# Performance work log

Measured on AMD Instinct MI355X. Metric: run time of the kernel, lower is better.

The kernel has to match this reference:

```python
import jax, jax.numpy as jnp
import numpy as np

N_NODES = 50000
N_EDGES = 800000
IN_FEAT = 128
HEADS = 4
UNITS = 16
LEAKY_ALPHA = 0.2  # tf.nn.leaky_relu default


def setup_inputs() -> dict:
    key = jax.random.key(0)
    k1, k2, k3, k4, k5 = jax.random.split(key, 5)
    x = jax.random.normal(k1, (N_NODES, IN_FEAT), dtype=jnp.float32)
    edge_index = jax.random.randint(k2, (N_EDGES, 2), 0, N_NODES, dtype=jnp.int32)
    # Dense kernel (glorot-ish scaling), no bias (use_bias=False)
    W = jax.random.normal(k3, (IN_FEAT, HEADS * UNITS), dtype=jnp.float32) * (1.0 / np.sqrt(IN_FEAT))
    glorot = np.sqrt(2.0 / (1 + UNITS)).astype(np.float32)
    att_w1 = jax.random.normal(k4, (HEADS, 1, UNITS), dtype=jnp.float32) * glorot
    att_w2 = jax.random.normal(k5, (HEADS, 1, UNITS), dtype=jnp.float32) * glorot
    return {"x": x, "edge_index": edge_index, "W": W, "att_w1": att_w1, "att_w2": att_w2}


def reference(x, edge_index, W, att_w1, att_w2):
    n_nodes = x.shape[0]
    h = x @ W  # [N, H*U]
    snd_idx = edge_index[:, 0]
    rcv_idx = edge_index[:, 1]
    # gather per-edge features, split into heads -> [H, E, U]
    sender = h[snd_idx].reshape(-1, HEADS, UNITS).transpose(1, 0, 2)
    receiver = h[rcv_idx].reshape(-1, HEADS, UNITS).transpose(1, 0, 2)
    # per-edge, per-head attention logits [H, E]
    att = jnp.sum(att_w1 * sender, axis=-1) + jnp.sum(att_w2 * receiver, axis=-1)
    att = jnp.where(att > 0, att, LEAKY_ALPHA * att)
    # segment softmax over receiver neighborhoods, per head
    seg_max = jax.vmap(lambda a: jax.ops.segment_max(a, rcv_idx, num_segments=n_nodes))(att)  # [H, N]
    e = jnp.exp(att - seg_max[:, rcv_idx])
    denom = jax.vmap(lambda a: jax.ops.segment_sum(a, rcv_idx, num_segments=n_nodes))(e)  # [H, N]
    alpha = e / denom[:, rcv_idx]  # [H, E]
    # weighted scatter-sum of sender features -> [H, N, U]
    out = jax.vmap(lambda v: jax.ops.segment_sum(v, rcv_idx, num_segments=n_nodes))(sender * alpha[:, :, None])
    # concat heads -> [N, H*U]; activation is None (identity)
    return out.transpose(1, 0, 2).reshape(n_nodes, HEADS * UNITS)
```

## Files before the change

kernel.cpp:

```cpp
#include <hip/hip_runtime.h>
#include <math.h>

#define N_NODES 50000
#define N_EDGES 800000
#define IN_FEAT 128
#define HEADS   4
#define UNITS   16
#define OUTF    64
#define LEAKY   0.2f

#define NB      196
#define BCAP    5120
#define CAP     64
#define GEMM_BLKS 782
#define A_BLOCKS  391
#define EPB     8

typedef __attribute__((ext_vector_type(8))) short bf16x8;
typedef __attribute__((ext_vector_type(4))) float f32x4;

__device__ __forceinline__ unsigned short f2bf(float f) {
    unsigned u = __float_as_uint(f);
    unsigned r = u + 0x7FFFu + ((u >> 16) & 1u);
    return (unsigned short)(r >> 16);
}
__device__ __forceinline__ float bf2f(unsigned short b) {
    return __uint_as_float(((unsigned)b) << 16);
}

union SharedU {
    struct { unsigned short wt[64 * 136]; } g;
    struct { int2 stage[2048]; int hist[256], cur[256], adj[256], wsum[4]; } a;
};

__global__ __launch_bounds__(256) void prep(const float* __restrict__ W,
                                            const float* __restrict__ w1,
                                            const float* __restrict__ w2,
                                            unsigned short* __restrict__ Wt_g,
                                            unsigned short* __restrict__ Wea_g,
                                            int* __restrict__ bucket_cnt) {
    int idx = blockIdx.x * 256 + threadIdx.x;
    if (idx < NB) bucket_cnt[idx] = 0;
    if (idx < IN_FEAT * OUTF) {
        int k = idx >> 6, c = idx & 63;
        Wt_g[c * IN_FEAT + k] = f2bf(W[idx]);
    }
    if (idx < IN_FEAT * HEADS) {
        int k = idx >> 2, hd = idx & 3;
        float s1 = 0.f, s2 = 0.f;
        #pragma unroll
        for (int u = 0; u < UNITS; ++u) {
            float wv = W[k * OUTF + hd * UNITS + u];
            s1 += wv * w1[hd * UNITS + u];
            s2 += wv * w2[hd * UNITS + u];
        }
        unsigned short h1 = f2bf(s1), h2 = f2bf(s2);
        unsigned short l1 = f2bf(s1 - bf2f(h1)), l2 = f2bf(s2 - bf2f(h2));
        Wea_g[(hd)      * IN_FEAT + k] = h1;
        Wea_g[(4 + hd)  * IN_FEAT + k] = h2;
        Wea_g[(8 + hd)  * IN_FEAT + k] = l1;
        Wea_g[(12 + hd) * IN_FEAT + k] = l2;
    }
}

__global__ __launch_bounds__(256, 4) void fused_gemm_bucketA(const float* __restrict__ x,
                                                             const unsigned short* __restrict__ Wt_g,
                                                             const unsigned short* __restrict__ Wea_g,
                                                             const int2* __restrict__ ei,
                                                             unsigned short* __restrict__ hg,
                                                             float* __restrict__ a1,
                                                             float* __restrict__ a2,
                                                             int* __restrict__ bucket_cnt,
                                                             int2* __restrict__ buckets) {
    __shared__ SharedU sh;
    const int t = threadIdx.x;
    const int lane = t & 63, wv = t >> 6;

    if (blockIdx.x >= GEMM_BLKS) {
        const int e0 = (blockIdx.x - GEMM_BLKS) * 2048;
        sh.a.hist[t] = 0;
        __syncthreads();

        int2 ed[EPB]; int bk[EPB];
        #pragma unroll
        for (int j = 0; j < EPB; ++j) {
            int e = e0 + t + j * 256;
            if (e < N_EDGES) {
                ed[j] = ei[e];
                bk[j] = ed[j].y >> 8;
                atomicAdd(&sh.a.hist[bk[j]], 1);
            } else bk[j] = -1;
        }
        __syncthreads();
        const int v = sh.a.hist[t];
        int inc = v;
        #pragma unroll
        for (int off = 1; off < 64; off <<= 1) {
            int u = __shfl_up(inc, off, 64);
            if (lane >= off) inc += u;
        }
        if (lane == 63) sh.a.wsum[wv] = inc;
        __syncthreads();
        const int s0 = sh.a.wsum[0], s1 = sh.a.wsum[1], s2 = sh.a.wsum[2];
        const int wo = (wv > 0 ? s0 : 0) + (wv > 1 ? s1 : 0) + (wv > 2 ? s2 : 0);
        const int excl = wo + inc - v;
        sh.a.cur[t] = excl;
        if (t < NB) {
            int g0 = atomicAdd(&bucket_cnt[t], v);
            sh.a.adj[t] = g0 - excl;
        }
        __syncthreads();
        #pragma unroll
        for (int j = 0; j < EPB; ++j) {
            if (bk[j] >= 0) {
                int p = atomicAdd(&sh.a.cur[bk[j]], 1);
                sh.a.stage[p] = ed[j];
            }
        }
        __syncthreads();
        const int total = min(2048, N_EDGES - e0);
        for (int i = t; i < total; i += 256) {
            int2 vv = sh.a.stage[i];
            int b = vv.y >> 8;
            buckets[(size_t)(b * BCAP + sh.a.adj[b] + i)] = vv;
        }
        return;
    }

    const int node0 = blockIdx.x * 64;
    unsigned short* wt = sh.g.wt;

    {
        const ushort4* Wt4 = (const ushort4*)Wt_g;
        #pragma unroll
        for (int it = 0; it < 8; ++it) {
            int idx = t + 256 * it;
            int c = idx >> 5, u = idx & 31;
            *(ushort4*)&wt[c * 136 + u * 4] = Wt4[idx];
        }
    }
    __syncthreads();

    const int m = lane & 15, quad = lane >> 4;
    const int n0 = wv * 16;
    const int arow = min(node0 + n0 + m, N_NODES - 1);
    const float* xr = x + (size_t)arow * IN_FEAT;

    f32x4 acc[4] = {{0,0,0,0},{0,0,0,0},{0,0,0,0},{0,0,0,0}};
    f32x4 acca   = {0,0,0,0};
    #pragma unroll
    for (int kc = 0; kc < 4; ++kc) {
        float4 v0 = *(const float4*)(xr + kc * 32 + quad * 8);
        float4 v1 = *(const float4*)(xr + kc * 32 + quad * 8 + 4);
        bf16x8 af;
        af[0] = (short)f2bf(v0.x); af[1] = (short)f2bf(v0.y);
        af[2] = (short)f2bf(v0.z); af[3] = (short)f2bf(v0.w);
        af[4] = (short)f2bf(v1.x); af[5] = (short)f2bf(v1.y);
        af[6] = (short)f2bf(v1.z); af[7] = (short)f2bf(v1.w);
        #pragma unroll
        for (int ct = 0; ct < 4; ++ct) {
            bf16x8 bfr = *(bf16x8*)&wt[(ct * 16 + m) * 136 + kc * 32 + quad * 8];
            acc[ct] = __builtin_amdgcn_mfma_f32_16x16x32_bf16(af, bfr, acc[ct], 0, 0, 0);
        }
        bf16x8 waf = *(const bf16x8*)(Wea_g + (size_t)m * IN_FEAT + kc * 32 + quad * 8);
        acca = __builtin_amdgcn_mfma_f32_16x16x32_bf16(af, waf, acca, 0, 0, 0);
    }

    #pragma unroll
    for (int r = 0; r < 4; ++r) {
        float vres = acca[r] + __shfl_xor(acca[r], 8, 64);
        int node = node0 + n0 + quad * 4 + r;
        if (node < N_NODES) {
            if (m < 4)      a1[node * 4 + m]       = vres;
            else if (m < 8) a2[node * 4 + (m - 4)] = vres;
        }
    }

    __syncthreads();
    unsigned short* hl = sh.g.wt;
    #pragma unroll
    for (int ct = 0; ct < 4; ++ct)
        #pragma unroll
        for (int r = 0; r < 4; ++r)
            hl[(n0 + quad * 4 + r) * 72 + ct * 16 + m] = f2bf(acc[ct][r]);
    __syncthreads();
    #pragma unroll
    for (int it = 0; it < 2; ++it) {
        int u = t + 256 * it;
        int r = u >> 3, cg = u & 7;
        int node = node0 + r;
        if (node < N_NODES)
            *(uint4*)&hg[(size_t)node * OUTF + cg * 8] = *(uint4*)&hl[r * 72 + cg * 8];
    }
}

__global__ __launch_bounds__(1024) void bucketB(const int2* __restrict__ buckets,
                                                const int* __restrict__ bucket_cnt,
                                                int* __restrict__ csr,
                                                int* __restrict__ deg) {
    __shared__ int snds[BCAP];
    __shared__ int hist[256], cur[256], strt[256], wsum[4];
    const int b = blockIdx.x;
    const int t = threadIdx.x;
    const int cnt = bucket_cnt[b];
    if (t < 256) hist[t] = 0;
    __syncthreads();
    for (int i = t; i < cnt; i += 1024)
        atomicAdd(&hist[buckets[(size_t)b * BCAP + i].y & 255], 1);
    __syncthreads();
    int v = 0, inc = 0;
    if (t < 256) {
        const int lane = t & 63, wvx = t >> 6;
        v = hist[t];
        inc = v;
        #pragma unroll
        for (int off = 1; off < 64; off <<= 1) {
            int u = __shfl_up(inc, off, 64);
            if (lane >= off) inc += u;
        }
        if (lane == 63) wsum[wvx] = inc;
    }
    __syncthreads();
    if (t < 256) {
        const int wvx = t >> 6;
        const int s0 = wsum[0], s1 = wsum[1], s2 = wsum[2];
        const int wo = (wvx > 0 ? s0 : 0) + (wvx > 1 ? s1 : 0) + (wvx > 2 ? s2 : 0);
        const int excl = wo + inc - v;
        strt[t] = excl;
        cur[t]  = excl;
        const int node = b * 256 + t;
        if (node < N_NODES) deg[node] = v;
    }
    __syncthreads();
    for (int i = t; i < cnt; i += 1024) {
        int2 vv = buckets[(size_t)b * BCAP + i];
        int p = atomicAdd(&cur[vv.y & 255], 1);
        snds[p] = vv.x;
    }
    __syncthreads();
    for (int u = t; u < 256 * CAP; u += 1024) {
        const int loc = u >> 6, slot = u & (CAP - 1);
        const int d = hist[loc];
        const int val = (d > 0) ? snds[strt[loc] + min(slot, d - 1)] : 0;
        csr[(size_t)b * (256 * CAP) + u] = val;
    }
}

__global__ __launch_bounds__(256, 8) void gather_kernel(const int* __restrict__ deg,
                                                        const int* __restrict__ csr,
                                                        const float* __restrict__ a1,
                                                        const float* __restrict__ a2,
                                                        const unsigned short* __restrict__ h,
                                                        float* __restrict__ out) {
    const int wave = threadIdx.x >> 6;
    const int lane = threadIdx.x & 63;
    const int n = blockIdx.x * 4 + wave;
    if (n >= N_NODES) return;
    const int sv = csr[(size_t)n * CAP + lane];
    const int cn = min(deg[n], CAP);
    const int sub  = lane >> 3;
    const int li   = lane & 7;
    const int head = li >> 1;
    if (cn <= 0) {
        if (sub == 0) {
            *(float4*)(out + (size_t)n * OUTF + li * 8)     = make_float4(0.f, 0.f, 0.f, 0.f);
            *(float4*)(out + (size_t)n * OUTF + li * 8 + 4) = make_float4(0.f, 0.f, 0.f, 0.f);
        }
        return;
    }
    const float a2h = a2[n * 4 + head];
    const uint4* h4 = (const uint4*)h;

    float acc[8] = {0.f,0.f,0.f,0.f,0.f,0.f,0.f,0.f};
    float den = 0.f;

    for (int i0 = 0; i0 < cn; i0 += 16) {
        #pragma unroll
        for (int g = 0; g < 2; ++g) {
            int er = i0 + g * 8 + sub;
            int ec = min(er, cn - 1);
            int s = __shfl(sv, ec, 64);
            float t0 = a1[s * 4 + head] + a2h;
            t0 = t0 > 0.f ? t0 : LEAKY * t0;
            float e = (er < cn) ? __expf(t0) : 0.f;
            uint4 hv = h4[(unsigned)(s * 8 + li)];
            const unsigned hw[4] = {hv.x, hv.y, hv.z, hv.w};
            #pragma unroll
            for (int q = 0; q < 4; ++q) {
                acc[q*2+0] = fmaf(e, __uint_as_float(hw[q] << 16),         acc[q*2+0]);
                acc[q*2+1] = fmaf(e, __uint_as_float(hw[q] & 0xFFFF0000u), acc[q*2+1]);
            }
            den += e;
        }
    }

    #pragma unroll
    for (int off = 8; off <= 32; off <<= 1) {
        #pragma unroll
        for (int q = 0; q < 8; ++q) acc[q] += __shfl_xor(acc[q], off, 64);
        den += __shfl_xor(den, off, 64);
    }

    if (sub == 0) {
        float inv = 1.f / den;
        *(float4*)(out + (size_t)n * OUTF + li * 8) =
            make_float4(acc[0] * inv, acc[1] * inv, acc[2] * inv, acc[3] * inv);
        *(float4*)(out + (size_t)n * OUTF + li * 8 + 4) =
            make_float4(acc[4] * inv, acc[5] * inv, acc[6] * inv, acc[7] * inv);
    }
}

extern "C" void kernel_launch(void* const* d_in, const int* in_sizes, int n_in,
                              void* d_out, int out_size, void* d_ws, size_t ws_size,
                              hipStream_t stream) {
    const float* x  = (const float*)d_in[0];
    const int2*  ei = (const int2*)d_in[1];
    const float* W  = (const float*)d_in[2];
    const float* w1 = (const float*)d_in[3];
    const float* w2 = (const float*)d_in[4];
    float* out = (float*)d_out;

    unsigned short* h    = (unsigned short*)d_ws;
    float* a1            = (float*)(h + (size_t)N_NODES * OUTF);
    float* a2            = a1 + (size_t)N_NODES * HEADS;
    unsigned short* Wt_g = (unsigned short*)(a2 + (size_t)N_NODES * HEADS);
    unsigned short* Wea_g = Wt_g + IN_FEAT * OUTF;
    int*   bucket_cnt    = (int*)(Wea_g + IN_FEAT * 16);
    int2*  buckets       = (int2*)(bucket_cnt + 256);
    int*   csr           = (int*)(buckets + (size_t)NB * BCAP);
    int*   deg           = csr + (size_t)NB * 256 * CAP;

    prep<<<32, 256, 0, stream>>>(W, w1, w2, Wt_g, Wea_g, bucket_cnt);
    fused_gemm_bucketA<<<GEMM_BLKS + A_BLOCKS, 256, 0, stream>>>(x, Wt_g, Wea_g, ei,
                                                                 h, a1, a2,
                                                                 bucket_cnt, buckets);
    bucketB<<<NB, 1024, 0, stream>>>(buckets, bucket_cnt, csr, deg);
    gather_kernel<<<(N_NODES + 3) / 4, 256, 0, stream>>>(deg, csr, a1, a2, h, out);
}
```

Measured before the change: 130.1 us.

## Pack edge pairs into 32 bits and store CSR neighbors as 16-bit ids

Each (sender, receiver) edge is packed into one 32-bit word, with the sender in the high 16 bits and the receiver in the low 16 bits. The padded CSR sender table now holds unsigned shorts. This halves the bytes written and read for the bucket array and the CSR table across the three kernels. Each bucketing block now handles 4096 edges with 16 edges per thread, so fewer blocks are launched. The scheme relies on node ids fitting in 16 bits, which holds for 50000 nodes but would break for graphs with more than 65535 nodes.

```diff
diff --git a/kernel.cpp b/kernel.cpp
--- a/kernel.cpp
+++ b/kernel.cpp
@@ -13,8 +13,8 @@
 #define BCAP    5120
 #define CAP     64
 #define GEMM_BLKS 782
-#define A_BLOCKS  391
-#define EPB     8
+#define A_BLOCKS  196
+#define EPB     16
 
 typedef __attribute__((ext_vector_type(8))) short bf16x8;
 typedef __attribute__((ext_vector_type(4))) float f32x4;
@@ -30,7 +30,7 @@
 
 union SharedU {
     struct { unsigned short wt[64 * 136]; } g;
-    struct { int2 stage[2048]; int hist[256], cur[256], adj[256], wsum[4]; } a;
+    struct { unsigned stage[4096]; int hist[256], cur[256], adj[256], wsum[4]; } a;
 };
 
 __global__ __launch_bounds__(256) void prep(const float* __restrict__ W,
@@ -71,23 +71,24 @@
                                                              float* __restrict__ a1,
                                                              float* __restrict__ a2,
                                                              int* __restrict__ bucket_cnt,
-                                                             int2* __restrict__ buckets) {
+                                                             unsigned* __restrict__ buckets) {
     __shared__ SharedU sh;
     const int t = threadIdx.x;
     const int lane = t & 63, wv = t >> 6;
 
     if (blockIdx.x >= GEMM_BLKS) {
-        const int e0 = (blockIdx.x - GEMM_BLKS) * 2048;
+        const int e0 = (blockIdx.x - GEMM_BLKS) * 4096;
         sh.a.hist[t] = 0;
         __syncthreads();
 
-        int2 ed[EPB]; int bk[EPB];
+        unsigned pk[EPB]; int bk[EPB];
         #pragma unroll
         for (int j = 0; j < EPB; ++j) {
             int e = e0 + t + j * 256;
             if (e < N_EDGES) {
-                ed[j] = ei[e];
-                bk[j] = ed[j].y >> 8;
+                int2 ed = ei[e];
+                pk[j] = ((unsigned)ed.x << 16) | (unsigned)ed.y;
+                bk[j] = ed.y >> 8;
                 atomicAdd(&sh.a.hist[bk[j]], 1);
             } else bk[j] = -1;
         }
@@ -114,14 +115,14 @@
         for (int j = 0; j < EPB; ++j) {
             if (bk[j] >= 0) {
                 int p = atomicAdd(&sh.a.cur[bk[j]], 1);
-                sh.a.stage[p] = ed[j];
+                sh.a.stage[p] = pk[j];
             }
         }
         __syncthreads();
-        const int total = min(2048, N_EDGES - e0);
+        const int total = min(4096, N_EDGES - e0);
         for (int i = t; i < total; i += 256) {
-            int2 vv = sh.a.stage[i];
-            int b = vv.y >> 8;
+            unsigned vv = sh.a.stage[i];
+            int b = (vv >> 8) & 255;
             buckets[(size_t)(b * BCAP + sh.a.adj[b] + i)] = vv;
         }
         return;
@@ -194,11 +195,11 @@
     }
 }
 
-__global__ __launch_bounds__(1024) void bucketB(const int2* __restrict__ buckets,
+__global__ __launch_bounds__(1024) void bucketB(const unsigned* __restrict__ buckets,
                                                 const int* __restrict__ bucket_cnt,
-                                                int* __restrict__ csr,
+                                                unsigned short* __restrict__ csr,
                                                 int* __restrict__ deg) {
-    __shared__ int snds[BCAP];
+    __shared__ unsigned short snds[BCAP];
     __shared__ int hist[256], cur[256], strt[256], wsum[4];
     const int b = blockIdx.x;
     const int t = threadIdx.x;
@@ -206,7 +207,7 @@
     if (t < 256) hist[t] = 0;
     __syncthreads();
     for (int i = t; i < cnt; i += 1024)
-        atomicAdd(&hist[buckets[(size_t)b * BCAP + i].y & 255], 1);
+        atomicAdd(&hist[buckets[(size_t)b * BCAP + i] & 255], 1);
     __syncthreads();
     int v = 0, inc = 0;
     if (t < 256) {
@@ -233,21 +234,21 @@
     }
     __syncthreads();
     for (int i = t; i < cnt; i += 1024) {
-        int2 vv = buckets[(size_t)b * BCAP + i];
-        int p = atomicAdd(&cur[vv.y & 255], 1);
-        snds[p] = vv.x;
+        unsigned vv = buckets[(size_t)b * BCAP + i];
+        int p = atomicAdd(&cur[vv & 255], 1);
+        snds[p] = (unsigned short)(vv >> 16);
     }
     __syncthreads();
     for (int u = t; u < 256 * CAP; u += 1024) {
         const int loc = u >> 6, slot = u & (CAP - 1);
         const int d = hist[loc];
-        const int val = (d > 0) ? snds[strt[loc] + min(slot, d - 1)] : 0;
+        const unsigned short val = (d > 0) ? snds[strt[loc] + min(slot, d - 1)] : 0;
         csr[(size_t)b * (256 * CAP) + u] = val;
     }
 }
 
 __global__ __launch_bounds__(256, 8) void gather_kernel(const int* __restrict__ deg,
-                                                        const int* __restrict__ csr,
+                                                        const unsigned short* __restrict__ csr,
                                                         const float* __restrict__ a1,
                                                         const float* __restrict__ a2,
                                                         const unsigned short* __restrict__ h,
@@ -326,9 +327,9 @@
     unsigned short* Wt_g = (unsigned short*)(a2 + (size_t)N_NODES * HEADS);
     unsigned short* Wea_g = Wt_g + IN_FEAT * OUTF;
     int*   bucket_cnt    = (int*)(Wea_g + IN_FEAT * 16);
-    int2*  buckets       = (int2*)(bucket_cnt + 256);
-    int*   csr           = (int*)(buckets + (size_t)NB * BCAP);
-    int*   deg           = csr + (size_t)NB * 256 * CAP;
+    unsigned* buckets    = (unsigned*)(bucket_cnt + 256);
+    unsigned short* csr  = (unsigned short*)(buckets + (size_t)NB * BCAP);
+    int*   deg           = (int*)(csr + (size_t)NB * 256 * CAP);
 
     prep<<<32, 256, 0, stream>>>(W, w1, w2, Wt_g, Wea_g, bucket_cnt);
     fused_gemm_bucketA<<<GEMM_BLKS + A_BLOCKS, 256, 0, stream>>>(x, Wt_g, Wea_g, ei,
```

New measurement: 126.1 us. 1.03x faster.
